# Kernel optimization log

Measured on AMD Instinct MI355X. Metric: run time of the kernel, lower is better.

Reference implementation:

```python
import jax, jax.numpy as jnp
import numpy as np

N = 128          # num_of_nodes
E = 4096         # directed edges (undirected doubled)
D = N + 2        # node feature dim after node_dim += num_of_nodes
H = 64           # hidden_dim


def _lin_params(key, fan_in, fan_out):
    s = 1.0 / np.sqrt(fan_in)
    kw, kb = jax.random.split(key)
    W = jax.random.uniform(kw, (fan_in, fan_out), jnp.float32, -s, s)
    b = jax.random.uniform(kb, (fan_out,), jnp.float32, -s, s)
    return W, b


def setup_inputs() -> dict:
    key = jax.random.key(0)
    ks = jax.random.split(key, 16)
    x = jax.random.normal(ks[0], (N, D), jnp.float32)
    edge_index = jax.random.randint(ks[1], (2, E), 0, N)
    edge_attr = jax.random.uniform(ks[2], (E, 1), jnp.float32)
    adjacency = jax.random.randint(ks[3], (N, N), 0, 2).astype(jnp.int32)
    # values in {-1, 0, 1}; -1 means node created no packet
    new_packets = jax.random.randint(ks[4], (N,), -1, 2).astype(jnp.float32)
    # conv1 edge MLP: Linear(1, D*H) -> ReLU -> Linear(D*H, D*H)
    W1a, b1a = _lin_params(ks[5], 1, D * H)
    W1b, b1b = _lin_params(ks[6], D * H, D * H)
    Wr1, _ = _lin_params(ks[7], D, H)        # NNConv root weight (no bias)
    bc1 = jnp.zeros((H,), jnp.float32)       # NNConv bias
    # conv2 edge MLP: Linear(1, H) -> ReLU -> Linear(H, H*H)
    W2a, b2a = _lin_params(ks[8], 1, H)
    W2b, b2b = _lin_params(ks[9], H, H * H)
    Wr2, _ = _lin_params(ks[10], H, H)
    bc2 = jnp.zeros((H,), jnp.float32)
    Wout, bout = _lin_params(ks[11], H, N)
    return dict(x=x, edge_index=edge_index, edge_attr=edge_attr,
                adjacency=adjacency, new_packets=new_packets,
                W1a=W1a, b1a=b1a, W1b=W1b, b1b=b1b, Wr1=Wr1, bc1=bc1,
                W2a=W2a, b2a=b2a, W2b=W2b, b2b=b2b, Wr2=Wr2, bc2=bc2,
                Wout=Wout, bout=bout)


def _nnconv(x, src, dst, edge_attr, Wa, ba, Wb, bb, Wr, bias, din, dout):
    # per-edge weight matrices from edge MLP: [E, din, dout]
    theta = (jax.nn.relu(edge_attr @ Wa + ba) @ Wb + bb).reshape(-1, din, dout)
    msg = jnp.einsum('ei,eio->eo', x[src], theta)          # gather + edge matmul
    agg = jax.ops.segment_sum(msg, dst, num_segments=N)     # scatter
    cnt = jax.ops.segment_sum(jnp.ones((msg.shape[0],), msg.dtype), dst,
                              num_segments=N)
    agg = agg / jnp.maximum(cnt, 1.0)[:, None]              # mean aggregation
    return agg + x @ Wr + bias                              # root weight + bias


def reference(x, edge_index, edge_attr, adjacency, new_packets,
              W1a, b1a, W1b, b1b, Wr1, bc1,
              W2a, b2a, W2b, b2b, Wr2, bc2,
              Wout, bout):
    src, dst = edge_index[0], edge_index[1]
    h = jax.nn.relu(_nnconv(x, src, dst, edge_attr, W1a, b1a, W1b, b1b, Wr1, bc1, D, H))
    h = jax.nn.relu(_nnconv(h, src, dst, edge_attr, W2a, b2a, W2b, b2b, Wr2, bc2, H, H))
    logits = h @ Wout + bout                                 # [N, N]
    masked = jnp.where(adjacency != 0, logits, -jnp.inf)
    probs = jax.nn.softmax(masked, axis=1)
    mask = new_packets != -1.0                               # nodes that created packets
    rp = jnp.where(mask[:, None], probs, 0.0)                # zero rows w/o packet
    idx = jnp.arange(N)
    rp = rp.at[idx, idx].add(jnp.where(mask, 0.0, 1.0))      # diag=1 for those rows
    return rp
```

## Files before the change

kernel.cpp:

```cpp
#include <hip/hip_runtime.h>

#define NN 128
#define NE 4096
#define DD 130
#define HH 64
#define KK1 8320
#define CC 256
#define NSEG 16
#define SEGC 16

#define OFF_AGG1 0
#define ZERO_F   8192
#define OFF_CNT  8192
#define OFF_XR1  8320
#define OFF_H1   16512
#define OFF_HB2  24704
#define OFF_HR2  32896
#define OFF_H2   41088
#define OFF_AGG2 49280
#define OFF_G2   57472
#define OFF_SP   581760
#define OFF_SQ   2711680
#define OFF_DP   4841600
#define OFF_DQ   6971520
#define OFF_INT  9101440
#define OFF_TP   9127040
#define OFF_TQ   9260160

__device__ __forceinline__ int event_bin(float a, float c) {
  if (a > 0.f) {
    if (c <= 0.f) { float tt = -c / a; if (tt < 1.f) return (int)(tt * 256.0f); }
  } else if (a < 0.f) {
    if (c > 0.f) { float tt = -c / a; if (tt < 1.f) return (int)ceilf(tt * 256.0f) - 1; }
  }
  return -1;
}

__global__ __launch_bounds__(256) void k_count(const int* __restrict__ ei,
                                               const float* __restrict__ eattr,
                                               const float* __restrict__ W1a,
                                               const float* __restrict__ b1a,
                                               int* __restrict__ e_off,
                                               int* __restrict__ k_off,
                                               int* __restrict__ e_idx,
                                               int* __restrict__ k_idx,
                                               int* __restrict__ base_idx,
                                               int* __restrict__ nbase,
                                               int* __restrict__ d_off,
                                               int* __restrict__ perm_dst,
                                               float* __restrict__ cnt) {
  __shared__ int ec[CC], kc[CC], cd[NN];
  __shared__ int eo[CC + 1], ko[CC + 1], doff[NN + 1];
  __shared__ int bcnt;
  int t = threadIdx.x;
  ec[t] = 0; kc[t] = 0;
  if (t < NN) cd[t] = 0;
  if (t == 0) bcnt = 0;
  __syncthreads();
  for (int e = t; e < NE; e += 256) {
    atomicAdd(&cd[ei[NE + e]], 1);
    int c = (int)(eattr[e] * 256.0f); c = c < 0 ? 0 : (c > CC - 1 ? CC - 1 : c);
    atomicAdd(&ec[c], 1);
  }
  for (int k = t; k < KK1; k += 256) {
    int b = event_bin(W1a[k], b1a[k]);
    if (b >= 0) atomicAdd(&kc[b], 1);
    if (b1a[k] > 0.f) { int p = atomicAdd(&bcnt, 1); base_idx[p] = k; }
  }
  __syncthreads();
  if (t == 0) {
    *nbase = bcnt;
    int r = 0;
    for (int c = 0; c < CC; c++) { eo[c] = r; r += ec[c]; } eo[CC] = r;
    r = 0;
    for (int c = 0; c < CC; c++) { ko[c] = r; r += kc[c]; } ko[CC] = r;
    r = 0;
    for (int n = 0; n < NN; n++) { doff[n] = r; r += cd[n]; } doff[NN] = r;
  }
  __syncthreads();
  if (t < NN) { cnt[t] = (float)cd[t]; d_off[t] = doff[t]; }
  if (t == 0) d_off[NN] = doff[NN];
  e_off[t] = eo[t]; k_off[t] = ko[t];
  if (t == 0) { e_off[CC] = eo[CC]; k_off[CC] = ko[CC]; }
  ec[t] = eo[t]; kc[t] = ko[t];
  if (t < NN) cd[t] = doff[t];
  __syncthreads();
  for (int e = t; e < NE; e += 256) {
    int c = (int)(eattr[e] * 256.0f); c = c < 0 ? 0 : (c > CC - 1 ? CC - 1 : c);
    int p = atomicAdd(&ec[c], 1);
    e_idx[p] = e;
    int d = ei[NE + e];
    int pd = atomicAdd(&cd[d], 1);
    perm_dst[pd] = e;
  }
  for (int k = t; k < KK1; k += 256) {
    int b = event_bin(W1a[k], b1a[k]);
    if (b >= 0) { int p = atomicAdd(&kc[b], 1); k_idx[p] = k; }
  }
}

__global__ __launch_bounds__(256) void k_small1x(const float* __restrict__ x,
                                                 const float* __restrict__ Wr1,
                                                 float* __restrict__ xr1) {
  int f = blockIdx.x * 256 + threadIdx.x;
  int n = f >> 6, o = f & 63;
  float a = 0.f;
  for (int i = 0; i < DD; i++) a = fmaf(x[n * DD + i], Wr1[i * HH + o], a);
  xr1[f] = a;
}

__global__ __launch_bounds__(256) void k_init(const float* __restrict__ b1b,
                                              float* __restrict__ SP0,
                                              float* __restrict__ SQ0) {
  int f = blockIdx.x * 256 + threadIdx.x;
  if (f < KK1) { SP0[f] = 0.f; SQ0[f] = b1b[f]; }
}

#define MCOL 33
__global__ __launch_bounds__(256) void k_base(const float* __restrict__ W1a,
                                              const float* __restrict__ b1a,
                                              const float* __restrict__ W1b,
                                              const int* __restrict__ base_idx,
                                              const int* __restrict__ nbase,
                                              float* __restrict__ SP0,
                                              float* __restrict__ SQ0) {
  int t = threadIdx.x;
  int nb = *nbase;
  float rp[MCOL], rq[MCOL];
#pragma unroll
  for (int m = 0; m < MCOL; m++) { rp[m] = 0.f; rq[m] = 0.f; }
  for (int r = blockIdx.x; r < nb; r += gridDim.x) {
    int k = base_idx[r];
    float a = W1a[k], c2 = b1a[k];
    const float* row = &W1b[(long)k * KK1];
#pragma unroll
    for (int m = 0; m < MCOL; m++) {
      int col = t + 256 * m;
      if (col < KK1) {
        float w = row[col];
        rp[m] = fmaf(a, w, rp[m]);
        rq[m] = fmaf(c2, w, rq[m]);
      }
    }
  }
#pragma unroll
  for (int m = 0; m < MCOL; m++) {
    int col = t + 256 * m;
    if (col < KK1) {
      atomicAdd(&SP0[col], rp[m]);
      atomicAdd(&SQ0[col], rq[m]);
    }
  }
}

__global__ __launch_bounds__(256) void k_diff(const float* __restrict__ W1a,
                                              const float* __restrict__ b1a,
                                              const float* __restrict__ W1b,
                                              const int* __restrict__ k_off,
                                              const int* __restrict__ k_idx,
                                              float* __restrict__ DP,
                                              float* __restrict__ DQ) {
  int c = blockIdx.x, t = threadIdx.x;
  int kb = k_off[c], ke = k_off[c + 1];
  float rp[MCOL], rq[MCOL];
#pragma unroll
  for (int m = 0; m < MCOL; m++) { rp[m] = 0.f; rq[m] = 0.f; }
  for (int r = kb; r < ke; ++r) {
    int k = k_idx[r];
    float a = W1a[k], c2 = b1a[k];
    float sa = (a > 0.f) ? a : -a;
    float sc = (a > 0.f) ? c2 : -c2;
    const float* row = &W1b[(long)k * KK1];
#pragma unroll
    for (int m = 0; m < MCOL; m++) {
      int col = t + 256 * m;
      if (col < KK1) {
        float w = row[col];
        rp[m] = fmaf(sa, w, rp[m]);
        rq[m] = fmaf(sc, w, rq[m]);
      }
    }
  }
#pragma unroll
  for (int m = 0; m < MCOL; m++) {
    int col = t + 256 * m;
    if (col < KK1) {
      DP[(long)c * KK1 + col] = rp[m];
      DQ[(long)c * KK1 + col] = rq[m];
    }
  }
}

__global__ __launch_bounds__(256) void k_seg(const float* __restrict__ DP,
                                             const float* __restrict__ DQ,
                                             float* __restrict__ TP,
                                             float* __restrict__ TQ) {
  int f = blockIdx.x * 256 + threadIdx.x;
  int s = blockIdx.y;
  const float* Dm; float* T; int col;
  if (f < KK1) { Dm = DP; T = TP; col = f; }
  else         { Dm = DQ; T = TQ; col = f - KK1; }
  float a = 0.f;
  for (int p = 0; p < SEGC; p++) a += Dm[(long)(s * SEGC + p) * KK1 + col];
  T[(long)s * KK1 + col] = a;
}

__global__ __launch_bounds__(256) void k_scan(float* __restrict__ SP,
                                              float* __restrict__ SQ,
                                              const float* __restrict__ DP,
                                              const float* __restrict__ DQ,
                                              const float* __restrict__ TP,
                                              const float* __restrict__ TQ) {
  int f = blockIdx.x * 256 + threadIdx.x;
  int s = blockIdx.y;
  float* S; const float* Dm; const float* T; int col;
  if (f < KK1) { S = SP; Dm = DP; T = TP; col = f; }
  else         { S = SQ; Dm = DQ; T = TQ; col = f - KK1; }
  float acc = S[col];
  for (int sp = 0; sp < s; sp++) acc += T[(long)sp * KK1 + col];
  for (int p = 0; p < SEGC; p++) {
    int c = s * SEGC + p;
    if (c > 0) S[(long)c * KK1 + col] = acc;
    acc += Dm[(long)c * KK1 + col];
  }
}

#define EC 192
#define KC 128
#define KHW 4160
__global__ __launch_bounds__(256) void k_sweep(const float* __restrict__ SP,
                                               const float* __restrict__ SQ,
                                               const float* __restrict__ W1a,
                                               const float* __restrict__ b1a,
                                               const float* __restrict__ W1b,
                                               const float* __restrict__ x,
                                               const float* __restrict__ eattr,
                                               const int* __restrict__ ei,
                                               const int* __restrict__ e_off,
                                               const int* __restrict__ e_idx,
                                               const int* __restrict__ k_off,
                                               const int* __restrict__ k_idx,
                                               float* __restrict__ agg1) {
  __shared__ float Pl[KHW], Ql[KHW];
  __shared__ float eas[EC], eas_r[EC];
  __shared__ int eix[EC], eix_r[EC];
  __shared__ float tks[KC], tks_r[KC];
  __shared__ int kix[KC], kix_r[KC];
  int c = blockIdx.x, oh = blockIdx.y, t = threadIdx.x;
  int ob = oh * 32;
  int eb = e_off[c], ne = e_off[c + 1] - eb; if (ne > EC) ne = EC;
  int kb = k_off[c], nk = k_off[c + 1] - kb; if (nk > KC) nk = KC;
  for (int j = t; j < KHW; j += 256) {
    int i = j >> 5, ol = j & 31;
    long col = (long)c * KK1 + i * 64 + ob + ol;
    Pl[j] = SP[col];
    Ql[j] = SQ[col];
  }
  if (t < ne) { int e = e_idx[eb + t]; eix_r[t] = e; eas_r[t] = eattr[e]; }
  if (t < nk) {
    int k = k_idx[kb + t];
    kix_r[t] = k;
    tks_r[t] = -b1a[k] / W1a[k];
  }
  __syncthreads();
  if (t < ne) {
    float key = eas_r[t]; int rk = 0;
    for (int j = 0; j < ne; j++) { float kj = eas_r[j]; rk += (kj < key) || (kj == key && j < t); }
    eas[rk] = key; eix[rk] = eix_r[t];
  }
  if (t < nk) {
    float key = tks_r[t]; int rk = 0;
    for (int j = 0; j < nk; j++) { float kj = tks_r[j]; rk += (kj < key) || (kj == key && j < t); }
    tks[rk] = key; kix[rk] = kix_r[t];
  }
  __syncthreads();
  if (ne == 0) return;
  int ie = 0, ik = 0;
  int q = t >> 5, ol = t & 31;
  while (ie < ne) {
    if (ik < nk && tks[ik] < eas[ie]) {
      int k = kix[ik];
      float a = W1a[k], c2 = b1a[k];
      float sa = (a > 0.f) ? a : -a;
      float sc = (a > 0.f) ? c2 : -c2;
      const float* row = &W1b[(long)k * KK1 + ob];
      __syncthreads();
      for (int j = t; j < KHW; j += 256) {
        int i = j >> 5, o2 = j & 31;
        float w = row[i * 64 + o2];
        Pl[j] = fmaf(sa, w, Pl[j]);
        Ql[j] = fmaf(sc, w, Ql[j]);
      }
      __syncthreads();
      ik++;
    } else {
      int m = 1;
      while (ie + m < ne && (ik >= nk || eas[ie + m] <= tks[ik])) m++;
      for (int g = 0; g < m; g += 8) {
        int sl = g + q;
        if (sl < m) {
          int e = eix[ie + sl];
          float eav = eas[ie + sl];
          int s = ei[e], d = ei[NE + e];
          const float* xp = &x[s * DD];
          float A = 0.f, B = 0.f;
#pragma unroll 2
          for (int i = 0; i < DD; i++) {
            float xv = xp[i];
            A = fmaf(xv, Pl[i * 32 + ol], A);
            B = fmaf(xv, Ql[i * 32 + ol], B);
          }
          atomicAdd(&agg1[d * 64 + ob + ol], fmaf(eav, A, B));
        }
      }
      ie += m;
    }
  }
}

__global__ __launch_bounds__(256) void k_h(const float* __restrict__ agg,
                                           const float* __restrict__ cnt,
                                           const float* __restrict__ xr,
                                           const float* __restrict__ bc,
                                           float* __restrict__ h) {
  int f = blockIdx.x * 256 + threadIdx.x;
  int n = f >> 6, o = f & 63;
  float c = fmaxf(cnt[n], 1.f);
  h[f] = fmaxf(0.f, agg[f] / c + xr[f] + bc[o]);
}

__global__ __launch_bounds__(256) void k_g2(const float* __restrict__ h1,
                                            const float* __restrict__ W2b,
                                            float* __restrict__ G2) {
  int f = blockIdx.x * 256 + threadIdx.x;
  int s = f >> 12, k = (f >> 6) & 63, o = f & 63;
  const float* hp = &h1[s * 64];
  const float* wp = &W2b[k * 4096 + o];
  float a = 0.f;
  for (int i = 0; i < 64; i++) a = fmaf(hp[i], wp[i * 64], a);
  G2[f] = a;
}

__global__ __launch_bounds__(256) void k_small2(const float* __restrict__ h1,
                                                const float* __restrict__ b2b,
                                                const float* __restrict__ Wr2,
                                                float* __restrict__ hb2,
                                                float* __restrict__ hr2) {
  int f = blockIdx.x * 256 + threadIdx.x;
  int n = f >> 6, o = f & 63;
  float a = 0.f, b = 0.f;
  for (int i = 0; i < 64; i++) {
    float hv = h1[n * 64 + i];
    a = fmaf(hv, b2b[i * 64 + o], a);
    b = fmaf(hv, Wr2[i * 64 + o], b);
  }
  hb2[f] = a; hr2[f] = b;
}

__global__ __launch_bounds__(256) void k_consume2(const float* __restrict__ G2,
                                                  const float* __restrict__ W2a,
                                                  const float* __restrict__ b2a,
                                                  const float* __restrict__ eattr,
                                                  const int* __restrict__ ei,
                                                  const int* __restrict__ d_off,
                                                  const int* __restrict__ perm_dst,
                                                  const float* __restrict__ hb2,
                                                  float* __restrict__ agg2) {
  __shared__ float wa[64], wb[64];
  __shared__ float red[8][32];
  int n = blockIdx.x, oh = blockIdx.y, t = threadIdx.x;
  int sl = t >> 5, ol = t & 31;
  if (t < 64) { wa[t] = W2a[t]; wb[t] = b2a[t]; }
  __syncthreads();
  int b0 = d_off[n], b1 = d_off[n + 1];
  float acc = 0.f;
  for (int r = b0 + sl; r < b1; r += 8) {
    int e = perm_dst[r];
    int s = ei[e];
    float ev = eattr[e];
    const float* gp = &G2[s * 4096 + oh * 32 + ol];
    float a = hb2[s * 64 + oh * 32 + ol];
    for (int k = 0; k < 64; k++) {
      float u = fmaxf(0.f, fmaf(ev, wa[k], wb[k]));
      a = fmaf(u, gp[k * 64], a);
    }
    acc += a;
  }
  red[sl][ol] = acc;
  __syncthreads();
  if (sl == 0) {
    float a = 0.f;
#pragma unroll
    for (int j = 0; j < 8; j++) a += red[j][ol];
    agg2[n * 64 + oh * 32 + ol] = a;
  }
}

__global__ __launch_bounds__(128) void k_out(const float* __restrict__ h2,
                                             const float* __restrict__ Wout,
                                             const float* __restrict__ bout,
                                             const int* __restrict__ adj,
                                             const float* __restrict__ npk,
                                             float* __restrict__ out) {
  __shared__ float hs[64];
  __shared__ float redm[2], reds[2];
  int n = blockIdx.x, j = threadIdx.x;
  if (j < 64) hs[j] = h2[n * 64 + j];
  __syncthreads();
  float l = bout[j];
  for (int k = 0; k < 64; k++) l = fmaf(hs[k], Wout[k * 128 + j], l);
  bool am = adj[n * 128 + j] != 0;
  float lm = am ? l : -3.0e38f;
  float m = lm;
  for (int off = 32; off >= 1; off >>= 1) m = fmaxf(m, __shfl_xor(m, off, 64));
  int wid = j >> 6;
  if ((j & 63) == 0) redm[wid] = m;
  __syncthreads();
  m = fmaxf(redm[0], redm[1]);
  float p = am ? expf(lm - m) : 0.f;
  float sv = p;
  for (int off = 32; off >= 1; off >>= 1) sv += __shfl_xor(sv, off, 64);
  if ((j & 63) == 0) reds[wid] = sv;
  __syncthreads();
  sv = reds[0] + reds[1];
  float prob = p / sv;
  bool haspkt = (npk[n] != -1.0f);
  out[n * 128 + j] = haspkt ? prob : ((j == n) ? 1.f : 0.f);
}

extern "C" void kernel_launch(void* const* d_in, const int* in_sizes, int n_in,
                              void* d_out, int out_size, void* d_ws, size_t ws_size,
                              hipStream_t stream) {
  const float* x    = (const float*)d_in[0];
  const int*   ei   = (const int*)  d_in[1];
  const float* ea   = (const float*)d_in[2];
  const int*   adj  = (const int*)  d_in[3];
  const float* npk  = (const float*)d_in[4];
  const float* W1a  = (const float*)d_in[5];
  const float* b1a  = (const float*)d_in[6];
  const float* W1b  = (const float*)d_in[7];
  const float* b1b  = (const float*)d_in[8];
  const float* Wr1  = (const float*)d_in[9];
  const float* bc1  = (const float*)d_in[10];
  const float* W2a  = (const float*)d_in[11];
  const float* b2a  = (const float*)d_in[12];
  const float* W2b  = (const float*)d_in[13];
  const float* b2b  = (const float*)d_in[14];
  const float* Wr2  = (const float*)d_in[15];
  const float* bc2  = (const float*)d_in[16];
  const float* Wout = (const float*)d_in[17];
  const float* bout = (const float*)d_in[18];

  float* ws = (float*)d_ws;
  int*   ip = (int*)(ws + OFF_INT);
  int* e_off    = ip;
  int* k_off    = ip + 257;
  int* e_idx    = ip + 514;
  int* k_idx    = ip + 4610;
  int* base_idx = ip + 12930;
  int* nbase    = ip + 21250;
  int* d_off    = ip + 21251;
  int* perm_dst = ip + 21380;

  hipMemsetAsync(ws + OFF_AGG1, 0, 8192 * sizeof(float), stream);

  k_count<<<1, 256, 0, stream>>>(ei, ea, W1a, b1a, e_off, k_off, e_idx, k_idx,
                                 base_idx, nbase, d_off, perm_dst, ws + OFF_CNT);
  k_small1x<<<32, 256, 0, stream>>>(x, Wr1, ws + OFF_XR1);
  k_init<<<33, 256, 0, stream>>>(b1b, ws + OFF_SP, ws + OFF_SQ);
  k_base<<<256, 256, 0, stream>>>(W1a, b1a, W1b, base_idx, nbase,
                                  ws + OFF_SP, ws + OFF_SQ);
  k_diff<<<CC, 256, 0, stream>>>(W1a, b1a, W1b, k_off, k_idx, ws + OFF_DP, ws + OFF_DQ);
  k_seg<<<dim3(65, NSEG), 256, 0, stream>>>(ws + OFF_DP, ws + OFF_DQ,
                                            ws + OFF_TP, ws + OFF_TQ);
  k_scan<<<dim3(65, NSEG), 256, 0, stream>>>(ws + OFF_SP, ws + OFF_SQ,
                                             ws + OFF_DP, ws + OFF_DQ,
                                             ws + OFF_TP, ws + OFF_TQ);
  k_sweep<<<dim3(CC, 2), 256, 0, stream>>>(ws + OFF_SP, ws + OFF_SQ, W1a, b1a, W1b,
                                           x, ea, ei, e_off, e_idx, k_off, k_idx,
                                           ws + OFF_AGG1);
  k_h<<<32, 256, 0, stream>>>(ws + OFF_AGG1, ws + OFF_CNT, ws + OFF_XR1, bc1, ws + OFF_H1);
  k_g2<<<2048, 256, 0, stream>>>(ws + OFF_H1, W2b, ws + OFF_G2);
  k_small2<<<32, 256, 0, stream>>>(ws + OFF_H1, b2b, Wr2, ws + OFF_HB2, ws + OFF_HR2);
  k_consume2<<<dim3(NN, 2), 256, 0, stream>>>(ws + OFF_G2, W2a, b2a, ea, ei,
                                              d_off, perm_dst, ws + OFF_HB2,
                                              ws + OFF_AGG2);
  k_h<<<32, 256, 0, stream>>>(ws + OFF_AGG2, ws + OFF_CNT, ws + OFF_HR2, bc2, ws + OFF_H2);
  k_out<<<128, 128, 0, stream>>>(ws + OFF_H2, Wout, bout, adj, npk, (float*)d_out);
}
```

Before: 643.9 us.

## Split sweep over input halves, write per-edge messages, and fuse small kernels

The conv1 sweep now splits the work by input-feature half instead of output half. Each block handles contiguous 4160-column slabs and writes per-edge partial messages to a buffer rather than doing atomic adds into agg1. A new gather kernel sums the two halves per destination using the CSR order, replacing the memset, the atomics and the cnt array. It also batches consecutive weight events in the sweep, makes k_base column-parallel over a 33x8 grid with scalar accumulators instead of 33-wide register arrays, and merges the small init/root and G2/small2 launches. The cost is an extra 2 MB message buffer that must be written and then read back.

```diff
diff --git a/kernel.cpp b/kernel.cpp
--- a/kernel.cpp
+++ b/kernel.cpp
@@ -8,24 +8,23 @@
 #define CC 256
 #define NSEG 16
 #define SEGC 16
-
-#define OFF_AGG1 0
-#define ZERO_F   8192
-#define OFF_CNT  8192
-#define OFF_XR1  8320
-#define OFF_H1   16512
-#define OFF_HB2  24704
-#define OFF_HR2  32896
-#define OFF_H2   41088
-#define OFF_AGG2 49280
-#define OFF_G2   57472
-#define OFF_SP   581760
-#define OFF_SQ   2711680
-#define OFF_DP   4841600
-#define OFF_DQ   6971520
-#define OFF_INT  9101440
-#define OFF_TP   9127040
-#define OFF_TQ   9260160
+#define KHW 4160
+
+#define OFF_XR1  0
+#define OFF_H1   8192
+#define OFF_HB2  16384
+#define OFF_HR2  24576
+#define OFF_H2   32768
+#define OFF_AGG2 40960
+#define OFF_G2   49152
+#define OFF_MSG  573440
+#define OFF_SP   1097728
+#define OFF_SQ   3227648
+#define OFF_DP   5357568
+#define OFF_DQ   7487488
+#define OFF_TP   9617408
+#define OFF_TQ   9750528
+#define OFF_INT  9883648
 
 __device__ __forceinline__ int event_bin(float a, float c) {
   if (a > 0.f) {
@@ -47,8 +46,7 @@
                                                int* __restrict__ base_idx,
                                                int* __restrict__ nbase,
                                                int* __restrict__ d_off,
-                                               int* __restrict__ perm_dst,
-                                               float* __restrict__ cnt) {
+                                               int* __restrict__ perm_dst) {
   __shared__ int ec[CC], kc[CC], cd[NN];
   __shared__ int eo[CC + 1], ko[CC + 1], doff[NN + 1];
   __shared__ int bcnt;
@@ -78,7 +76,7 @@
     for (int n = 0; n < NN; n++) { doff[n] = r; r += cd[n]; } doff[NN] = r;
   }
   __syncthreads();
-  if (t < NN) { cnt[t] = (float)cd[t]; d_off[t] = doff[t]; }
+  if (t < NN) d_off[t] = doff[t];
   if (t == 0) d_off[NN] = doff[NN];
   e_off[t] = eo[t]; k_off[t] = ko[t];
   if (t == 0) { e_off[CC] = eo[CC]; k_off[CC] = ko[CC]; }
@@ -99,24 +97,22 @@
   }
 }
 
-__global__ __launch_bounds__(256) void k_small1x(const float* __restrict__ x,
-                                                 const float* __restrict__ Wr1,
-                                                 float* __restrict__ xr1) {
-  int f = blockIdx.x * 256 + threadIdx.x;
-  int n = f >> 6, o = f & 63;
-  float a = 0.f;
-  for (int i = 0; i < DD; i++) a = fmaf(x[n * DD + i], Wr1[i * HH + o], a);
-  xr1[f] = a;
-}
-
-__global__ __launch_bounds__(256) void k_init(const float* __restrict__ b1b,
-                                              float* __restrict__ SP0,
-                                              float* __restrict__ SQ0) {
+__global__ __launch_bounds__(256) void k_pre(const float* __restrict__ b1b,
+                                             const float* __restrict__ x,
+                                             const float* __restrict__ Wr1,
+                                             float* __restrict__ SP0,
+                                             float* __restrict__ SQ0,
+                                             float* __restrict__ xr1) {
   int f = blockIdx.x * 256 + threadIdx.x;
   if (f < KK1) { SP0[f] = 0.f; SQ0[f] = b1b[f]; }
-}
-
-#define MCOL 33
+  if (f < NN * HH) {
+    int n = f >> 6, o = f & 63;
+    float a = 0.f;
+    for (int i = 0; i < DD; i++) a = fmaf(x[n * DD + i], Wr1[i * HH + o], a);
+    xr1[f] = a;
+  }
+}
+
 __global__ __launch_bounds__(256) void k_base(const float* __restrict__ W1a,
                                               const float* __restrict__ b1a,
                                               const float* __restrict__ W1b,
@@ -124,35 +120,24 @@
                                               const int* __restrict__ nbase,
                                               float* __restrict__ SP0,
                                               float* __restrict__ SQ0) {
-  int t = threadIdx.x;
+  int col = blockIdx.x * 256 + threadIdx.x;
+  bool valid = col < KK1;
   int nb = *nbase;
-  float rp[MCOL], rq[MCOL];
-#pragma unroll
-  for (int m = 0; m < MCOL; m++) { rp[m] = 0.f; rq[m] = 0.f; }
-  for (int r = blockIdx.x; r < nb; r += gridDim.x) {
+  float rp = 0.f, rq = 0.f;
+  for (int r = blockIdx.y; r < nb; r += 8) {
     int k = base_idx[r];
     float a = W1a[k], c2 = b1a[k];
-    const float* row = &W1b[(long)k * KK1];
-#pragma unroll
-    for (int m = 0; m < MCOL; m++) {
-      int col = t + 256 * m;
-      if (col < KK1) {
-        float w = row[col];
-        rp[m] = fmaf(a, w, rp[m]);
-        rq[m] = fmaf(c2, w, rq[m]);
-      }
-    }
-  }
-#pragma unroll
-  for (int m = 0; m < MCOL; m++) {
-    int col = t + 256 * m;
-    if (col < KK1) {
-      atomicAdd(&SP0[col], rp[m]);
-      atomicAdd(&SQ0[col], rq[m]);
-    }
-  }
-}
-
+    float w = valid ? W1b[(long)k * KK1 + col] : 0.f;
+    rp = fmaf(a, w, rp);
+    rq = fmaf(c2, w, rq);
+  }
+  if (valid) {
+    atomicAdd(&SP0[col], rp);
+    atomicAdd(&SQ0[col], rq);
+  }
+}
+
+#define MCOL 33
 __global__ __launch_bounds__(256) void k_diff(const float* __restrict__ W1a,
                                               const float* __restrict__ b1a,
                                               const float* __restrict__ W1b,
@@ -227,7 +212,6 @@
 
 #define EC 192
 #define KC 128
-#define KHW 4160
 __global__ __launch_bounds__(256) void k_sweep(const float* __restrict__ SP,
                                                const float* __restrict__ SQ,
                                                const float* __restrict__ W1a,
@@ -240,21 +224,19 @@
                                                const int* __restrict__ e_idx,
                                                const int* __restrict__ k_off,
                                                const int* __restrict__ k_idx,
-                                               float* __restrict__ agg1) {
+                                               float* __restrict__ msg) {
   __shared__ float Pl[KHW], Ql[KHW];
   __shared__ float eas[EC], eas_r[EC];
   __shared__ int eix[EC], eix_r[EC];
   __shared__ float tks[KC], tks_r[KC];
   __shared__ int kix[KC], kix_r[KC];
-  int c = blockIdx.x, oh = blockIdx.y, t = threadIdx.x;
-  int ob = oh * 32;
+  int c = blockIdx.x, ih = blockIdx.y, t = threadIdx.x;
+  int jb = ih * KHW;
   int eb = e_off[c], ne = e_off[c + 1] - eb; if (ne > EC) ne = EC;
   int kb = k_off[c], nk = k_off[c + 1] - kb; if (nk > KC) nk = KC;
   for (int j = t; j < KHW; j += 256) {
-    int i = j >> 5, ol = j & 31;
-    long col = (long)c * KK1 + i * 64 + ob + ol;
-    Pl[j] = SP[col];
-    Ql[j] = SQ[col];
+    Pl[j] = SP[(long)c * KK1 + jb + j];
+    Ql[j] = SQ[(long)c * KK1 + jb + j];
   }
   if (t < ne) { int e = e_idx[eb + t]; eix_r[t] = e; eas_r[t] = eattr[e]; }
   if (t < nk) {
@@ -276,85 +258,96 @@
   __syncthreads();
   if (ne == 0) return;
   int ie = 0, ik = 0;
-  int q = t >> 5, ol = t & 31;
+  int q = t >> 6, o = t & 63;
+  float* mbase = msg + (long)ih * (NE * 64);
   while (ie < ne) {
-    if (ik < nk && tks[ik] < eas[ie]) {
-      int k = kix[ik];
-      float a = W1a[k], c2 = b1a[k];
-      float sa = (a > 0.f) ? a : -a;
-      float sc = (a > 0.f) ? c2 : -c2;
-      const float* row = &W1b[(long)k * KK1 + ob];
+    int me = 0;
+    while (ik + me < nk && tks[ik + me] < eas[ie]) me++;
+    if (me > 0) {
       __syncthreads();
-      for (int j = t; j < KHW; j += 256) {
-        int i = j >> 5, o2 = j & 31;
-        float w = row[i * 64 + o2];
-        Pl[j] = fmaf(sa, w, Pl[j]);
-        Ql[j] = fmaf(sc, w, Ql[j]);
+      for (int ev = 0; ev < me; ev++) {
+        int k = kix[ik + ev];
+        float a = W1a[k], c2 = b1a[k];
+        float sa = (a > 0.f) ? a : -a;
+        float sc = (a > 0.f) ? c2 : -c2;
+        const float* row = &W1b[(long)k * KK1 + jb];
+        for (int j = t; j < KHW; j += 256) {
+          float w = row[j];
+          Pl[j] = fmaf(sa, w, Pl[j]);
+          Ql[j] = fmaf(sc, w, Ql[j]);
+        }
       }
       __syncthreads();
-      ik++;
-    } else {
-      int m = 1;
-      while (ie + m < ne && (ik >= nk || eas[ie + m] <= tks[ik])) m++;
-      for (int g = 0; g < m; g += 8) {
-        int sl = g + q;
-        if (sl < m) {
-          int e = eix[ie + sl];
-          float eav = eas[ie + sl];
-          int s = ei[e], d = ei[NE + e];
-          const float* xp = &x[s * DD];
-          float A = 0.f, B = 0.f;
-#pragma unroll 2
-          for (int i = 0; i < DD; i++) {
-            float xv = xp[i];
-            A = fmaf(xv, Pl[i * 32 + ol], A);
-            B = fmaf(xv, Ql[i * 32 + ol], B);
-          }
-          atomicAdd(&agg1[d * 64 + ob + ol], fmaf(eav, A, B));
+      ik += me;
+    }
+    int m = 1;
+    while (ie + m < ne && (ik >= nk || eas[ie + m] <= tks[ik])) m++;
+    for (int g = 0; g < m; g += 4) {
+      int sl = g + q;
+      if (sl < m) {
+        int e = eix[ie + sl];
+        float eav = eas[ie + sl];
+        int s = ei[e];
+        const float* xp = &x[s * DD + ih * 65];
+        float A = 0.f, B = 0.f;
+#pragma unroll 5
+        for (int i = 0; i < 65; i++) {
+          float xv = xp[i];
+          A = fmaf(xv, Pl[i * 64 + o], A);
+          B = fmaf(xv, Ql[i * 64 + o], B);
         }
+        mbase[e * 64 + o] = fmaf(eav, A, B);
       }
-      ie += m;
-    }
-  }
-}
-
-__global__ __launch_bounds__(256) void k_h(const float* __restrict__ agg,
-                                           const float* __restrict__ cnt,
-                                           const float* __restrict__ xr,
-                                           const float* __restrict__ bc,
-                                           float* __restrict__ h) {
+    }
+    ie += m;
+  }
+}
+
+__global__ __launch_bounds__(256) void k_aggh(const float* __restrict__ msg,
+                                              const int* __restrict__ d_off,
+                                              const int* __restrict__ perm_dst,
+                                              const float* __restrict__ xr1,
+                                              const float* __restrict__ bc1,
+                                              float* __restrict__ h1) {
   int f = blockIdx.x * 256 + threadIdx.x;
   int n = f >> 6, o = f & 63;
-  float c = fmaxf(cnt[n], 1.f);
-  h[f] = fmaxf(0.f, agg[f] / c + xr[f] + bc[o]);
-}
-
-__global__ __launch_bounds__(256) void k_g2(const float* __restrict__ h1,
-                                            const float* __restrict__ W2b,
-                                            float* __restrict__ G2) {
-  int f = blockIdx.x * 256 + threadIdx.x;
-  int s = f >> 12, k = (f >> 6) & 63, o = f & 63;
-  const float* hp = &h1[s * 64];
-  const float* wp = &W2b[k * 4096 + o];
-  float a = 0.f;
-  for (int i = 0; i < 64; i++) a = fmaf(hp[i], wp[i * 64], a);
-  G2[f] = a;
-}
-
-__global__ __launch_bounds__(256) void k_small2(const float* __restrict__ h1,
-                                                const float* __restrict__ b2b,
-                                                const float* __restrict__ Wr2,
-                                                float* __restrict__ hb2,
-                                                float* __restrict__ hr2) {
-  int f = blockIdx.x * 256 + threadIdx.x;
-  int n = f >> 6, o = f & 63;
-  float a = 0.f, b = 0.f;
-  for (int i = 0; i < 64; i++) {
-    float hv = h1[n * 64 + i];
-    a = fmaf(hv, b2b[i * 64 + o], a);
-    b = fmaf(hv, Wr2[i * 64 + o], b);
-  }
-  hb2[f] = a; hr2[f] = b;
+  int b0 = d_off[n], b1 = d_off[n + 1];
+  float v = 0.f;
+  for (int r = b0; r < b1; r++) {
+    int e = perm_dst[r];
+    v += msg[e * 64 + o] + msg[NE * 64 + e * 64 + o];
+  }
+  float cn = fmaxf((float)(b1 - b0), 1.f);
+  h1[f] = fmaxf(0.f, v / cn + xr1[f] + bc1[o]);
+}
+
+__global__ __launch_bounds__(256) void k_g2s(const float* __restrict__ h1,
+                                             const float* __restrict__ W2b,
+                                             const float* __restrict__ b2b,
+                                             const float* __restrict__ Wr2,
+                                             float* __restrict__ G2,
+                                             float* __restrict__ hb2,
+                                             float* __restrict__ hr2) {
+  int bx = blockIdx.x, t = threadIdx.x;
+  if (bx < 2048) {
+    int f = bx * 256 + t;
+    int s = f >> 12, k = (f >> 6) & 63, o = f & 63;
+    const float* hp = &h1[s * 64];
+    const float* wp = &W2b[k * 4096 + o];
+    float a = 0.f;
+    for (int i = 0; i < 64; i++) a = fmaf(hp[i], wp[i * 64], a);
+    G2[f] = a;
+  } else {
+    int f = (bx - 2048) * 256 + t;
+    int n = f >> 6, o = f & 63;
+    float a = 0.f, b = 0.f;
+    for (int i = 0; i < 64; i++) {
+      float hv = h1[n * 64 + i];
+      a = fmaf(hv, b2b[i * 64 + o], a);
+      b = fmaf(hv, Wr2[i * 64 + o], b);
+    }
+    hb2[f] = a; hr2[f] = b;
+  }
 }
 
 __global__ __launch_bounds__(256) void k_consume2(const float* __restrict__ G2,
@@ -394,6 +387,17 @@
     for (int j = 0; j < 8; j++) a += red[j][ol];
     agg2[n * 64 + oh * 32 + ol] = a;
   }
+}
+
+__global__ __launch_bounds__(256) void k_h2d(const float* __restrict__ agg,
+                                             const int* __restrict__ d_off,
+                                             const float* __restrict__ xr,
+                                             const float* __restrict__ bc,
+                                             float* __restrict__ h) {
+  int f = blockIdx.x * 256 + threadIdx.x;
+  int n = f >> 6, o = f & 63;
+  float c = fmaxf((float)(d_off[n + 1] - d_off[n]), 1.f);
+  h[f] = fmaxf(0.f, agg[f] / c + xr[f] + bc[o]);
 }
 
 __global__ __launch_bounds__(128) void k_out(const float* __restrict__ h2,
@@ -462,14 +466,11 @@
   int* d_off    = ip + 21251;
   int* perm_dst = ip + 21380;
 
-  hipMemsetAsync(ws + OFF_AGG1, 0, 8192 * sizeof(float), stream);
-
   k_count<<<1, 256, 0, stream>>>(ei, ea, W1a, b1a, e_off, k_off, e_idx, k_idx,
-                                 base_idx, nbase, d_off, perm_dst, ws + OFF_CNT);
-  k_small1x<<<32, 256, 0, stream>>>(x, Wr1, ws + OFF_XR1);
-  k_init<<<33, 256, 0, stream>>>(b1b, ws + OFF_SP, ws + OFF_SQ);
-  k_base<<<256, 256, 0, stream>>>(W1a, b1a, W1b, base_idx, nbase,
-                                  ws + OFF_SP, ws + OFF_SQ);
+                                 base_idx, nbase, d_off, perm_dst);
+  k_pre<<<33, 256, 0, stream>>>(b1b, x, Wr1, ws + OFF_SP, ws + OFF_SQ, ws + OFF_XR1);
+  k_base<<<dim3(33, 8), 256, 0, stream>>>(W1a, b1a, W1b, base_idx, nbase,
+                                          ws + OFF_SP, ws + OFF_SQ);
   k_diff<<<CC, 256, 0, stream>>>(W1a, b1a, W1b, k_off, k_idx, ws + OFF_DP, ws + OFF_DQ);
   k_seg<<<dim3(65, NSEG), 256, 0, stream>>>(ws + OFF_DP, ws + OFF_DQ,
                                             ws + OFF_TP, ws + OFF_TQ);
@@ -478,13 +479,14 @@
                                              ws + OFF_TP, ws + OFF_TQ);
   k_sweep<<<dim3(CC, 2), 256, 0, stream>>>(ws + OFF_SP, ws + OFF_SQ, W1a, b1a, W1b,
                                            x, ea, ei, e_off, e_idx, k_off, k_idx,
-                                           ws + OFF_AGG1);
-  k_h<<<32, 256, 0, stream>>>(ws + OFF_AGG1, ws + OFF_CNT, ws + OFF_XR1, bc1, ws + OFF_H1);
-  k_g2<<<2048, 256, 0, stream>>>(ws + OFF_H1, W2b, ws + OFF_G2);
-  k_small2<<<32, 256, 0, stream>>>(ws + OFF_H1, b2b, Wr2, ws + OFF_HB2, ws + OFF_HR2);
+                                           ws + OFF_MSG);
+  k_aggh<<<32, 256, 0, stream>>>(ws + OFF_MSG, d_off, perm_dst, ws + OFF_XR1, bc1,
+                                 ws + OFF_H1);
+  k_g2s<<<2080, 256, 0, stream>>>(ws + OFF_H1, W2b, b2b, Wr2,
+                                  ws + OFF_G2, ws + OFF_HB2, ws + OFF_HR2);
   k_consume2<<<dim3(NN, 2), 256, 0, stream>>>(ws + OFF_G2, W2a, b2a, ea, ei,
                                               d_off, perm_dst, ws + OFF_HB2,
                                               ws + OFF_AGG2);
-  k_h<<<32, 256, 0, stream>>>(ws + OFF_AGG2, ws + OFF_CNT, ws + OFF_HR2, bc2, ws + OFF_H2);
+  k_h2d<<<32, 256, 0, stream>>>(ws + OFF_AGG2, d_off, ws + OFF_HR2, bc2, ws + OFF_H2);
   k_out<<<128, 128, 0, stream>>>(ws + OFF_H2, Wout, bout, adj, npk, (float*)d_out);
 }
```

New measurement: 827.3 us. 1.28x slower.
